# Performance work log

Measured on AMD Instinct MI355X. Metric: run time of the kernel, lower is better.

Reference implementation:

```python
import jax, jax.numpy as jnp
import numpy as np

NUM_ITEMS = 50000
EMB = 16
SLATE = 10
HID = 512
LAT = 64
RESP = 1024
BATCH = 256


def _linear_params(k, out_dim, in_dim):
    kw, kb = jax.random.split(k)
    s = 1.0 / np.sqrt(in_dim)
    W = jax.random.uniform(kw, (out_dim, in_dim), jnp.float32, -s, s)
    b = jax.random.uniform(kb, (out_dim,), jnp.float32, -s, s)
    return W, b


def setup_inputs() -> dict:
    key = jax.random.key(0)
    ks = jax.random.split(key, 10)
    user_repr = jax.random.randint(ks[0], (BATCH, NUM_ITEMS), 0, 2, dtype=jnp.int32)
    slate = jax.random.randint(ks[1], (BATCH, SLATE), 0, NUM_ITEMS, dtype=jnp.int32)
    response_encoded = jax.random.uniform(ks[2], (BATCH, RESP), jnp.float32)
    eps = jax.random.normal(ks[3], (BATCH, LAT), jnp.float32)
    emb = jax.random.normal(ks[4], (NUM_ITEMS, EMB), jnp.float32)
    in_enc = SLATE * EMB + EMB + RESP
    W_enc, b_enc = _linear_params(ks[5], HID, in_enc)
    W_mu, b_mu = _linear_params(ks[6], LAT, HID)
    W_lv, b_lv = _linear_params(ks[7], LAT, HID)
    in_dec = LAT + EMB + RESP
    W_d1, b_d1 = _linear_params(ks[8], HID, in_dec)
    W_d2, b_d2 = _linear_params(ks[9], SLATE * EMB, HID)
    return {"user_repr": user_repr, "slate": slate, "response_encoded": response_encoded,
            "eps": eps, "emb": emb, "W_enc": W_enc, "b_enc": b_enc,
            "W_mu": W_mu, "b_mu": b_mu, "W_lv": W_lv, "b_lv": b_lv,
            "W_d1": W_d1, "b_d1": b_d1, "W_d2": W_d2, "b_d2": b_d2}


def reference(user_repr, slate, response_encoded, eps, emb,
              W_enc, b_enc, W_mu, b_mu, W_lv, b_lv, W_d1, b_d1, W_d2, b_d2):
    # Ragged embedding-mean pooling over interacted items (vectorized segment mean):
    # mean of emb rows where user_repr==1  ==  (indicator @ emb) / count
    uf = user_repr.astype(jnp.float32)                       # [B, N]
    counts = jnp.sum(uf, axis=1, keepdims=True)              # [B, 1]
    user = (uf @ emb) / counts                               # [B, E]

    cond = jnp.concatenate([user, response_encoded], axis=1)  # [B, E+R]
    slate_emb = emb[slate]                                    # [B, K, E]
    slate_vec = slate_emb.reshape(-1, SLATE * EMB)            # [B, K*E]
    x = jnp.concatenate([slate_vec, cond], axis=1)

    # encoder
    h = jax.nn.relu(x @ W_enc.T + b_enc)
    z_mean = h @ W_mu.T + b_mu
    z_log_var = h @ W_lv.T + b_lv

    # reparameterized sample
    z = z_mean + eps * jnp.exp(0.5 * z_log_var)

    # decoder
    dz = jnp.concatenate([z, cond], axis=1)
    dh = jax.nn.relu(dz @ W_d1.T + b_d1)
    rx = jax.nn.relu(dh @ W_d2.T + b_d2)                      # [B, K*E]
    rx = rx.reshape(-1, SLATE, EMB)                           # [B, K, E]

    # scores vs all items, softmax over items
    logits = jnp.einsum('bkh,nh->bkn', rx, emb)               # [B, K, N]
    probs = jax.nn.softmax(logits, axis=2)
    recon_slate = jnp.argmax(probs, axis=2)                   # [B, K]
    recon_resp = jnp.take_along_axis(probs, slate[:, :, None], axis=2)[..., 0]  # [B, K]
    return z_mean, z_log_var, recon_slate, recon_resp
```

## Files before the change

### kernel.cpp

```cpp
#include <hip/hip_runtime.h>

#define NITEMS 50000
#define EMBD   16
#define NSLATE 10
#define HIDD   512
#define LATD   64
#define RESPD  1024
#define BATCH  256
#define NPCH   10
#define PI4    1250
#define BG     4
#define LOG2E  1.44269504088896340736f
#define SHIFT  64.0f

#define NCOL   2560
#define NT     1563
#define IC     128
#define TPC    13

#define OUT_ZM 0
#define OUT_ZLV 16384
#define OUT_RS 32768
#define OUT_RR 35328

#define WS_X    0
#define WS_DZ   307200
#define WS_P2   0
#define WS_PS   0
#define WS_PM   327680
#define WS_PA   655360
#define WS_PP   589824
#define WS_PART 589824
#define WS_RX   1114112
#define WS_RXS0 1155072
#define WS_RXS1 1175552
#define WS_RXS2 1196032

typedef __attribute__((ext_vector_type(8))) short bfrag;
typedef __attribute__((ext_vector_type(16))) float f32x16;

__device__ __forceinline__ float bfround(float v) {
  unsigned u = __float_as_uint(v);
  unsigned r = (u + 0x7FFFu + ((u >> 16) & 1u)) & 0xFFFF0000u;
  return __uint_as_float(r);
}

__global__ __launch_bounds__(256) void pool_part(const int* __restrict__ u,
    const float* __restrict__ emb, float* __restrict__ pp) {
  int bg = blockIdx.x, c = blockIdx.y, t = threadIdx.x;
  float acc[BG][17];
  #pragma unroll
  for (int j = 0; j < BG; ++j)
    #pragma unroll
    for (int i = 0; i < 17; ++i) acc[j][i] = 0.0f;
  const int4* ub = (const int4*)u;
  size_t base = (size_t)(bg * BG) * 12500 + (size_t)c * PI4;
  int nBase = c * 5000;
  for (int i4 = t; i4 < PI4; i4 += 256) {
    int4 u0 = ub[base + i4];
    int4 u1 = ub[base + 12500 + i4];
    int4 u2 = ub[base + 25000 + i4];
    int4 u3 = ub[base + 37500 + i4];
    int w[BG][4] = {{u0.x, u0.y, u0.z, u0.w}, {u1.x, u1.y, u1.z, u1.w},
                    {u2.x, u2.y, u2.z, u2.w}, {u3.x, u3.y, u3.z, u3.w}};
    const float4* e4 = (const float4*)(emb + (size_t)(nBase + i4 * 4) * 16);
    #pragma unroll
    for (int it = 0; it < 4; ++it) {
      float4 ea = e4[it * 4 + 0], eb = e4[it * 4 + 1];
      float4 ec = e4[it * 4 + 2], ed = e4[it * 4 + 3];
      #pragma unroll
      for (int j = 0; j < BG; ++j) {
        float wf = (float)w[j][it];
        acc[j][0]  = fmaf(wf, ea.x, acc[j][0]);
        acc[j][1]  = fmaf(wf, ea.y, acc[j][1]);
        acc[j][2]  = fmaf(wf, ea.z, acc[j][2]);
        acc[j][3]  = fmaf(wf, ea.w, acc[j][3]);
        acc[j][4]  = fmaf(wf, eb.x, acc[j][4]);
        acc[j][5]  = fmaf(wf, eb.y, acc[j][5]);
        acc[j][6]  = fmaf(wf, eb.z, acc[j][6]);
        acc[j][7]  = fmaf(wf, eb.w, acc[j][7]);
        acc[j][8]  = fmaf(wf, ec.x, acc[j][8]);
        acc[j][9]  = fmaf(wf, ec.y, acc[j][9]);
        acc[j][10] = fmaf(wf, ec.z, acc[j][10]);
        acc[j][11] = fmaf(wf, ec.w, acc[j][11]);
        acc[j][12] = fmaf(wf, ed.x, acc[j][12]);
        acc[j][13] = fmaf(wf, ed.y, acc[j][13]);
        acc[j][14] = fmaf(wf, ed.z, acc[j][14]);
        acc[j][15] = fmaf(wf, ed.w, acc[j][15]);
        acc[j][16] += wf;
      }
    }
  }
  #pragma unroll
  for (int off = 32; off > 0; off >>= 1) {
    #pragma unroll
    for (int j = 0; j < BG; ++j)
      #pragma unroll
      for (int i = 0; i < 17; ++i) acc[j][i] += __shfl_down(acc[j][i], off);
  }
  int lane = t & 63, wv = t >> 6;
  if (lane == 0) {
    float* dst = pp + (size_t)((bg * NPCH + c) * 4 + wv) * (BG * 17);
    #pragma unroll
    for (int j = 0; j < BG; ++j)
      #pragma unroll
      for (int i = 0; i < 17; ++i) dst[j * 17 + i] = acc[j][i];
  }
}

__global__ __launch_bounds__(256) void build_x(const float* __restrict__ pp,
    const int* __restrict__ slate, const float* __restrict__ resp,
    const float* __restrict__ emb, float* __restrict__ x, float* __restrict__ dz) {
  __shared__ float fin[17];
  int b = blockIdx.x, t = threadIdx.x;
  if (t < 17) {
    int bg = b >> 2, j = b & 3;
    float a = 0.f;
    const float* p = pp + (size_t)(bg * NPCH * 4) * (BG * 17) + j * 17 + t;
    #pragma unroll
    for (int w = 0; w < NPCH * 4; ++w) a += p[(size_t)w * (BG * 17)];
    fin[t] = a;
  }
  __syncthreads();
  float inv = 1.0f / fin[16];
  if (t < 16) {
    float uv = fin[t] * inv;
    x[b * 1200 + 160 + t] = uv;
    dz[b * 1104 + 64 + t] = uv;
  }
  if (t >= 32 && t < 192) {
    int i = t - 32;
    int k = i >> 4, e = i & 15;
    int it = slate[b * 10 + k];
    x[b * 1200 + i] = emb[(size_t)it * 16 + e];
  }
  for (int i = t; i < 1024; i += 256) {
    float r = resp[b * 1024 + i];
    x[b * 1200 + 176 + i] = r;
    dz[b * 1104 + 80 + i] = r;
  }
}

__global__ __launch_bounds__(256) void gemm64(const float* __restrict__ A,
    const float* __restrict__ B, float* __restrict__ P, int M, int N, int K, int kChunk) {
  __shared__ float As[16][68];
  __shared__ float Bs[16][68];
  int tid = threadIdx.x;
  int m0 = blockIdx.y * 64, n0 = blockIdx.x * 64;
  int ks = blockIdx.z * kChunk;
  int ke = ks + kChunk; if (ke > K) ke = K;
  int sr = tid >> 2;
  int sc = (tid & 3) * 4;
  int tx = tid & 15, ty = tid >> 4;
  float acc[4][4];
  #pragma unroll
  for (int i = 0; i < 4; ++i)
    #pragma unroll
    for (int j = 0; j < 4; ++j) acc[i][j] = 0.f;
  for (int k0 = ks; k0 < ke; k0 += 16) {
    float4 av = make_float4(0.f, 0.f, 0.f, 0.f);
    float4 bv = make_float4(0.f, 0.f, 0.f, 0.f);
    if (k0 + sc < ke)
      av = *(const float4*)(A + (size_t)(m0 + sr) * K + k0 + sc);
    if (k0 + sc < ke && n0 + sr < N)
      bv = *(const float4*)(B + (size_t)(n0 + sr) * K + k0 + sc);
    __syncthreads();
    As[sc][sr] = av.x; As[sc + 1][sr] = av.y; As[sc + 2][sr] = av.z; As[sc + 3][sr] = av.w;
    Bs[sc][sr] = bv.x; Bs[sc + 1][sr] = bv.y; Bs[sc + 2][sr] = bv.z; Bs[sc + 3][sr] = bv.w;
    __syncthreads();
    #pragma unroll
    for (int kk = 0; kk < 16; ++kk) {
      float4 a4 = *(const float4*)&As[kk][4 * ty];
      float4 b4 = *(const float4*)&Bs[kk][4 * tx];
      float a[4] = {a4.x, a4.y, a4.z, a4.w};
      float b[4] = {b4.x, b4.y, b4.z, b4.w};
      #pragma unroll
      for (int i = 0; i < 4; ++i)
        #pragma unroll
        for (int j = 0; j < 4; ++j) acc[i][j] = fmaf(a[i], b[j], acc[i][j]);
    }
  }
  float* Pz = P + (size_t)blockIdx.z * M * N;
  #pragma unroll
  for (int i = 0; i < 4; ++i) {
    int m = m0 + 4 * ty + i, n = n0 + 4 * tx;
    if (n < N)
      *(float4*)(Pz + (size_t)m * N + n) = make_float4(acc[i][0], acc[i][1], acc[i][2], acc[i][3]);
  }
}

__global__ __launch_bounds__(128) void mulv_z_kernel(const float* __restrict__ part,
    const float* __restrict__ benc,
    const float* __restrict__ Wmu, const float* __restrict__ bmu,
    const float* __restrict__ Wlv, const float* __restrict__ blv,
    const float* __restrict__ eps, float* __restrict__ out, float* __restrict__ dz) {
  __shared__ __align__(16) float hs[512];
  __shared__ float zms[64], zlvs[64];
  int b = blockIdx.x, t = threadIdx.x;
  for (int i = t; i < 512; i += 128) {
    float a = benc[i];
    #pragma unroll
    for (int s = 0; s < 4; ++s) a += part[(size_t)s * 131072 + b * 512 + i];
    hs[i] = fmaxf(a, 0.f);
  }
  __syncthreads();
  const float* Wr = (t < 64) ? (Wmu + (size_t)t * 512) : (Wlv + (size_t)(t - 64) * 512);
  float bias = (t < 64) ? bmu[t] : blv[t - 64];
  const float4* w4 = (const float4*)Wr;
  const float4* h4 = (const float4*)hs;
  float a0 = 0.f, a1 = 0.f, a2 = 0.f, a3 = 0.f;
  #pragma unroll 4
  for (int i = 0; i < 128; ++i) {
    float4 w = w4[i], hv = h4[i];
    a0 = fmaf(w.x, hv.x, a0); a1 = fmaf(w.y, hv.y, a1);
    a2 = fmaf(w.z, hv.z, a2); a3 = fmaf(w.w, hv.w, a3);
  }
  float acc = (a0 + a1) + (a2 + a3) + bias;
  if (t < 64) { out[OUT_ZM + b * 64 + t] = acc; zms[t] = acc; }
  else        { out[OUT_ZLV + b * 64 + (t - 64)] = acc; zlvs[t - 64] = acc; }
  __syncthreads();
  if (t < 64) {
    float zv = fmaf(eps[b * 64 + t], __builtin_amdgcn_exp2f(0.7213475204444817f * zlvs[t]), zms[t]);
    dz[b * 1104 + t] = zv;
  }
}

__global__ __launch_bounds__(256) void gemm_d2(const float* __restrict__ part,
    const float* __restrict__ bd1, const float* __restrict__ W, float* __restrict__ p2) {
  __shared__ float As[16][68];
  __shared__ float Bs[16][68];
  const int N = 160;
  int tid = threadIdx.x;
  int m0 = blockIdx.y * 64, n0 = blockIdx.x * 64;
  int ks = blockIdx.z * 64, ke = ks + 64;
  int sr = tid >> 2, sc = (tid & 3) * 4;
  int tx = tid & 15, ty = tid >> 4;
  float acc[4][4];
  #pragma unroll
  for (int i = 0; i < 4; ++i)
    #pragma unroll
    for (int j = 0; j < 4; ++j) acc[i][j] = 0.f;
  for (int k0 = ks; k0 < ke; k0 += 16) {
    int col = k0 + sc;
    const float* p = part + (size_t)(m0 + sr) * 512 + col;
    float4 a0 = *(const float4*)(p);
    float4 a1 = *(const float4*)(p + 131072);
    float4 a2 = *(const float4*)(p + 262144);
    float4 a3 = *(const float4*)(p + 393216);
    float4 bb = *(const float4*)(bd1 + col);
    float4 av;
    av.x = fmaxf(a0.x + a1.x + a2.x + a3.x + bb.x, 0.f);
    av.y = fmaxf(a0.y + a1.y + a2.y + a3.y + bb.y, 0.f);
    av.z = fmaxf(a0.z + a1.z + a2.z + a3.z + bb.z, 0.f);
    av.w = fmaxf(a0.w + a1.w + a2.w + a3.w + bb.w, 0.f);
    float4 bv = make_float4(0.f, 0.f, 0.f, 0.f);
    if (n0 + sr < N)
      bv = *(const float4*)(W + (size_t)(n0 + sr) * 512 + col);
    __syncthreads();
    As[sc][sr] = av.x; As[sc + 1][sr] = av.y; As[sc + 2][sr] = av.z; As[sc + 3][sr] = av.w;
    Bs[sc][sr] = bv.x; Bs[sc + 1][sr] = bv.y; Bs[sc + 2][sr] = bv.z; Bs[sc + 3][sr] = bv.w;
    __syncthreads();
    #pragma unroll
    for (int kk = 0; kk < 16; ++kk) {
      float4 a4 = *(const float4*)&As[kk][4 * ty];
      float4 b4 = *(const float4*)&Bs[kk][4 * tx];
      float a[4] = {a4.x, a4.y, a4.z, a4.w};
      float b[4] = {b4.x, b4.y, b4.z, b4.w};
      #pragma unroll
      for (int i = 0; i < 4; ++i)
        #pragma unroll
        for (int j = 0; j < 4; ++j) acc[i][j] = fmaf(a[i], b[j], acc[i][j]);
    }
  }
  float* Pz = p2 + (size_t)blockIdx.z * 40960;
  #pragma unroll
  for (int i = 0; i < 4; ++i) {
    int m = m0 + 4 * ty + i, n = n0 + 4 * tx;
    if (n < N)
      *(float4*)(Pz + (size_t)m * 160 + n) = make_float4(acc[i][0], acc[i][1], acc[i][2], acc[i][3]);
  }
}

__global__ __launch_bounds__(256) void rx_prep(const float* __restrict__ p2,
    const float* __restrict__ bd2, float* __restrict__ rx,
    unsigned short* __restrict__ rx0, unsigned short* __restrict__ rx1,
    unsigned short* __restrict__ rx2) {
  int b = blockIdx.x, t = threadIdx.x;
  if (t >= 160) return;
  float a = bd2[t];
  #pragma unroll
  for (int z = 0; z < 8; ++z) a += p2[(size_t)z * 40960 + b * 160 + t];
  float v = fmaxf(a, 0.f) * LOG2E;
  rx[b * 160 + t] = v;
  int col = b * 10 + (t >> 4), e = t & 15;
  float f0 = bfround(v);
  float d1 = v - f0;
  float f1 = bfround(d1);
  float d2 = d1 - f1;
  float f2 = bfround(d2);
  rx0[col * 16 + e] = (unsigned short)(__float_as_uint(f0) >> 16);
  rx1[col * 16 + e] = (unsigned short)(__float_as_uint(f1) >> 16);
  rx2[col * 16 + e] = (unsigned short)(__float_as_uint(f2) >> 16);
}

__global__ __launch_bounds__(256) void score_mfma(const float* __restrict__ emb,
    const unsigned short* __restrict__ rx0, const unsigned short* __restrict__ rx1,
    const unsigned short* __restrict__ rx2,
    float* __restrict__ ps, float* __restrict__ pm, int* __restrict__ pa) {
  int t = threadIdx.x;
  int w = t >> 6, l = t & 63;
  int ln = l & 31, hf = l >> 5;
  int pair = blockIdx.x * 4 + w;
  int ic = blockIdx.y;
  int colA = pair * 64 + ln;
  int colB = colA + 32;
  size_t offA = (size_t)colA * 16 + hf * 8;
  size_t offB = (size_t)colB * 16 + hf * 8;
  bfrag bA0 = *(const bfrag*)(rx0 + offA);
  bfrag bA1 = *(const bfrag*)(rx1 + offA);
  bfrag bA2 = *(const bfrag*)(rx2 + offA);
  bfrag bB0 = *(const bfrag*)(rx0 + offB);
  bfrag bB1 = *(const bfrag*)(rx1 + offB);
  bfrag bB2 = *(const bfrag*)(rx2 + offB);
  float sA = 0.f, sB = 0.f;
  float mA = -3.402823466e38f, mB = -3.402823466e38f;
  int aA = 0x7FFFFFFF, aB = 0x7FFFFFFF;
  int ts = ic * TPC, te = ts + TPC;
  if (te > NT) te = NT;
  #pragma unroll 1
  for (int tile = ts; tile < te; ++tile) {
    int r = tile * 32 + ln;
    float4 e0, e1;
    if (r < NITEMS) {
      const float4* p = (const float4*)(emb + (size_t)r * 16 + hf * 8);
      e0 = p[0]; e1 = p[1];
    } else {
      e0 = make_float4(-128.f, -128.f, -128.f, -128.f);
      e1 = e0;
    }
    float ev[8] = {e0.x, e0.y, e0.z, e0.w, e1.x, e1.y, e1.z, e1.w};
    union { bfrag f; unsigned u[4]; } A0, A1, A2;
    #pragma unroll
    for (int j = 0; j < 4; ++j) {
      float v0 = ev[2 * j], v1 = ev[2 * j + 1];
      unsigned u0 = __float_as_uint(v0), u1 = __float_as_uint(v1);
      A0.u[j] = (u0 >> 16) | (u1 & 0xFFFF0000u);
      float r0 = v0 - __uint_as_float(u0 & 0xFFFF0000u);
      float r1 = v1 - __uint_as_float(u1 & 0xFFFF0000u);
      unsigned w0 = __float_as_uint(r0), w1 = __float_as_uint(r1);
      A1.u[j] = (w0 >> 16) | (w1 & 0xFFFF0000u);
      float q0 = r0 - __uint_as_float(w0 & 0xFFFF0000u);
      float q1 = r1 - __uint_as_float(w1 & 0xFFFF0000u);
      A2.u[j] = (__float_as_uint(q0) >> 16) | (__float_as_uint(q1) & 0xFFFF0000u);
    }
    f32x16 accA, accB;
    #pragma unroll
    for (int i = 0; i < 16; ++i) { accA[i] = -SHIFT; accB[i] = -SHIFT; }
    accA = __builtin_amdgcn_mfma_f32_32x32x16_bf16(A1.f, bA1, accA, 0, 0, 0);
    accB = __builtin_amdgcn_mfma_f32_32x32x16_bf16(A1.f, bB1, accB, 0, 0, 0);
    accA = __builtin_amdgcn_mfma_f32_32x32x16_bf16(A2.f, bA0, accA, 0, 0, 0);
    accB = __builtin_amdgcn_mfma_f32_32x32x16_bf16(A2.f, bB0, accB, 0, 0, 0);
    accA = __builtin_amdgcn_mfma_f32_32x32x16_bf16(A0.f, bA2, accA, 0, 0, 0);
    accB = __builtin_amdgcn_mfma_f32_32x32x16_bf16(A0.f, bB2, accB, 0, 0, 0);
    accA = __builtin_amdgcn_mfma_f32_32x32x16_bf16(A1.f, bA0, accA, 0, 0, 0);
    accB = __builtin_amdgcn_mfma_f32_32x32x16_bf16(A1.f, bB0, accB, 0, 0, 0);
    accA = __builtin_amdgcn_mfma_f32_32x32x16_bf16(A0.f, bA1, accA, 0, 0, 0);
    accB = __builtin_amdgcn_mfma_f32_32x32x16_bf16(A0.f, bB1, accB, 0, 0, 0);
    accA = __builtin_amdgcn_mfma_f32_32x32x16_bf16(A0.f, bA0, accA, 0, 0, 0);
    accB = __builtin_amdgcn_mfma_f32_32x32x16_bf16(A0.f, bB0, accB, 0, 0, 0);
    int base = tile * 32 + 4 * hf;
    #pragma unroll
    for (int g = 0; g < 4; ++g) {
      #pragma unroll
      for (int q = 0; q < 4; ++q) {
        int idx = base + 8 * g + q;
        float xa = accA[g * 4 + q];
        sA += __builtin_amdgcn_exp2f(xa);
        if (xa > mA) { mA = xa; aA = idx; }
        float xb = accB[g * 4 + q];
        sB += __builtin_amdgcn_exp2f(xb);
        if (xb > mB) { mB = xb; aB = idx; }
      }
    }
  }
  sA += __shfl_xor(sA, 32);
  sB += __shfl_xor(sB, 32);
  float omA = __shfl_xor(mA, 32); int oaA = __shfl_xor(aA, 32);
  if (omA > mA || (omA == mA && oaA < aA)) { mA = omA; aA = oaA; }
  float omB = __shfl_xor(mB, 32); int oaB = __shfl_xor(aB, 32);
  if (omB > mB || (omB == mB && oaB < aB)) { mB = omB; aB = oaB; }
  if (hf == 0) {
    int idxA = ic * NCOL + colA;
    int idxB = ic * NCOL + colB;
    ps[idxA] = sA; pm[idxA] = mA; pa[idxA] = aA;
    ps[idxB] = sB; pm[idxB] = mB; pa[idxB] = aB;
  }
}

__global__ __launch_bounds__(256) void score_final(const float* __restrict__ psg,
    const float* __restrict__ pmg, const int* __restrict__ pag,
    const float* __restrict__ rx, const float* __restrict__ emb,
    const int* __restrict__ slate, float* __restrict__ out) {
  int tid = blockIdx.x * 256 + threadIdx.x;
  if (tid >= BATCH * 10) return;
  int b = tid / 10, k = tid % 10;
  float S = 0.f, M = -3.402823466e38f;
  int AM = 2147483647;
  for (int c = 0; c < IC; ++c) {
    int idx = c * NCOL + tid;
    S += psg[idx];
    float m2 = pmg[idx];
    int oa = pag[idx];
    bool take = (m2 > M) || (m2 == M && oa < AM);
    AM = take ? oa : AM;
    M = fmaxf(M, m2);
  }
  int it = slate[b * 10 + k];
  const float* er = emb + (size_t)it * 16;
  const float* rr = rx + b * 160 + k * 16;
  float xs = -SHIFT;
  #pragma unroll
  for (int e = 0; e < 16; ++e) xs = fmaf(rr[e], er[e], xs);
  out[OUT_RS + b * 10 + k] = (float)AM;
  out[OUT_RR + b * 10 + k] = __builtin_amdgcn_exp2f(xs) / S;
}

extern "C" void kernel_launch(void* const* d_in, const int* in_sizes, int n_in,
                              void* d_out, int out_size, void* d_ws, size_t ws_size,
                              hipStream_t stream) {
  const int* user_repr = (const int*)d_in[0];
  const int* slate = (const int*)d_in[1];
  const float* resp = (const float*)d_in[2];
  const float* eps = (const float*)d_in[3];
  const float* emb = (const float*)d_in[4];
  const float* W_enc = (const float*)d_in[5];
  const float* b_enc = (const float*)d_in[6];
  const float* W_mu = (const float*)d_in[7];
  const float* b_mu = (const float*)d_in[8];
  const float* W_lv = (const float*)d_in[9];
  const float* b_lv = (const float*)d_in[10];
  const float* W_d1 = (const float*)d_in[11];
  const float* b_d1 = (const float*)d_in[12];
  const float* W_d2 = (const float*)d_in[13];
  const float* b_d2 = (const float*)d_in[14];
  float* out = (float*)d_out;
  float* ws = (float*)d_ws;

  float* x    = ws + WS_X;
  float* dz   = ws + WS_DZ;
  float* p2   = ws + WS_P2;
  float* pp   = ws + WS_PP;
  float* part = ws + WS_PART;
  float* ps   = ws + WS_PS;
  float* pmb  = ws + WS_PM;
  int*   pab  = (int*)(ws + WS_PA);
  float* rx   = ws + WS_RX;
  unsigned short* rx0 = (unsigned short*)(ws + WS_RXS0);
  unsigned short* rx1 = (unsigned short*)(ws + WS_RXS1);
  unsigned short* rx2 = (unsigned short*)(ws + WS_RXS2);

  pool_part<<<dim3(64, NPCH), 256, 0, stream>>>(user_repr, emb, pp);
  build_x<<<256, 256, 0, stream>>>(pp, slate, resp, emb, x, dz);
  gemm64<<<dim3(8, 4, 4), 256, 0, stream>>>(x, W_enc, part, 256, 512, 1200, 300);
  mulv_z_kernel<<<256, 128, 0, stream>>>(part, b_enc, W_mu, b_mu, W_lv, b_lv, eps, out, dz);
  gemm64<<<dim3(8, 4, 4), 256, 0, stream>>>(dz, W_d1, part, 256, 512, 1104, 276);
  gemm_d2<<<dim3(3, 4, 8), 256, 0, stream>>>(part, b_d1, W_d2, p2);
  rx_prep<<<256, 256, 0, stream>>>(p2, b_d2, rx, rx0, rx1, rx2);
  score_mfma<<<dim3(10, IC), 256, 0, stream>>>(emb, rx0, rx1, rx2, ps, pmb, pab);
  score_final<<<10, 256, 0, stream>>>(ps, pmb, pab, rx, emb, slate, out);
}
```

Baseline: 276.1 us.

## Track per-tile max in scoring loop and recover argmax in a fix-up kernel

The score kernel now keeps only the running max value and the tile index that produced it, using a branch-free fmax tree per tile, instead of tracking an element index per element. Per-column results are merged across chunks with 64-bit atomicMax on a packed key of the order-preserving max and the tile index. A new argmax_fix kernel recomputes the winning tile with MFMA to find the exact item index. The item-dimension split also grows from 128 to 224 chunks to raise parallelism. In exchange it adds an extra launch, global atomics, and key zeroing inside rx_prep.

New measurement: 273.0 us. Within noise of the previous version (-1.1%).

```diff
diff --git a/kernel.cpp b/kernel.cpp
--- a/kernel.cpp
+++ b/kernel.cpp
@@ -15,8 +15,8 @@
 
 #define NCOL   2560
 #define NT     1563
-#define IC     128
-#define TPC    13
+#define IC     224
+#define TPC    7
 
 #define OUT_ZM 0
 #define OUT_ZLV 16384
@@ -27,8 +27,7 @@
 #define WS_DZ   307200
 #define WS_P2   0
 #define WS_PS   0
-#define WS_PM   327680
-#define WS_PA   655360
+#define WS_KEY  573440
 #define WS_PP   589824
 #define WS_PART 589824
 #define WS_RX   1114112
@@ -44,6 +43,13 @@
   unsigned r = (u + 0x7FFFu + ((u >> 16) & 1u)) & 0xFFFF0000u;
   return __uint_as_float(r);
 }
+
+__device__ __forceinline__ unsigned mono32(float f) {
+  unsigned u = __float_as_uint(f);
+  return (u & 0x80000000u) ? ~u : (u | 0x80000000u);
+}
+
+#define FMAX3(a, b, c) fmaxf(fmaxf((a), (b)), (c))
 
 __global__ __launch_bounds__(256) void pool_part(const int* __restrict__ u,
     const float* __restrict__ emb, float* __restrict__ pp) {
@@ -284,8 +290,9 @@
 __global__ __launch_bounds__(256) void rx_prep(const float* __restrict__ p2,
     const float* __restrict__ bd2, float* __restrict__ rx,
     unsigned short* __restrict__ rx0, unsigned short* __restrict__ rx1,
-    unsigned short* __restrict__ rx2) {
+    unsigned short* __restrict__ rx2, unsigned long long* __restrict__ keys) {
   int b = blockIdx.x, t = threadIdx.x;
+  if (t < 10) keys[b * 10 + t] = 0ULL;
   if (t >= 160) return;
   float a = bd2[t];
   #pragma unroll
@@ -306,7 +313,7 @@
 __global__ __launch_bounds__(256) void score_mfma(const float* __restrict__ emb,
     const unsigned short* __restrict__ rx0, const unsigned short* __restrict__ rx1,
     const unsigned short* __restrict__ rx2,
-    float* __restrict__ ps, float* __restrict__ pm, int* __restrict__ pa) {
+    float* __restrict__ ps, unsigned long long* __restrict__ keys) {
   int t = threadIdx.x;
   int w = t >> 6, l = t & 63;
   int ln = l & 31, hf = l >> 5;
@@ -324,7 +331,7 @@
   bfrag bB2 = *(const bfrag*)(rx2 + offB);
   float sA = 0.f, sB = 0.f;
   float mA = -3.402823466e38f, mB = -3.402823466e38f;
-  int aA = 0x7FFFFFFF, aB = 0x7FFFFFFF;
+  int tlA = 0, tlB = 0;
   int ts = ic * TPC, te = ts + TPC;
   if (te > NT) te = NT;
   #pragma unroll 1
@@ -368,60 +375,140 @@
     accB = __builtin_amdgcn_mfma_f32_32x32x16_bf16(A0.f, bB1, accB, 0, 0, 0);
     accA = __builtin_amdgcn_mfma_f32_32x32x16_bf16(A0.f, bA0, accA, 0, 0, 0);
     accB = __builtin_amdgcn_mfma_f32_32x32x16_bf16(A0.f, bB0, accB, 0, 0, 0);
-    int base = tile * 32 + 4 * hf;
-    #pragma unroll
-    for (int g = 0; g < 4; ++g) {
-      #pragma unroll
-      for (int q = 0; q < 4; ++q) {
-        int idx = base + 8 * g + q;
-        float xa = accA[g * 4 + q];
-        sA += __builtin_amdgcn_exp2f(xa);
-        if (xa > mA) { mA = xa; aA = idx; }
-        float xb = accB[g * 4 + q];
-        sB += __builtin_amdgcn_exp2f(xb);
-        if (xb > mB) { mB = xb; aB = idx; }
-      }
+    float tmA, tmB;
+    {
+      float f1 = FMAX3(accA[0], accA[1], accA[2]);
+      float f2 = FMAX3(accA[3], accA[4], accA[5]);
+      float f3 = FMAX3(accA[6], accA[7], accA[8]);
+      float f4 = FMAX3(accA[9], accA[10], accA[11]);
+      float f5 = FMAX3(accA[12], accA[13], accA[14]);
+      float g1 = FMAX3(f1, f2, accA[15]);
+      float g2 = fmaxf(f3, f4);
+      tmA = FMAX3(g1, g2, f5);
+    }
+    {
+      float f1 = FMAX3(accB[0], accB[1], accB[2]);
+      float f2 = FMAX3(accB[3], accB[4], accB[5]);
+      float f3 = FMAX3(accB[6], accB[7], accB[8]);
+      float f4 = FMAX3(accB[9], accB[10], accB[11]);
+      float f5 = FMAX3(accB[12], accB[13], accB[14]);
+      float g1 = FMAX3(f1, f2, accB[15]);
+      float g2 = fmaxf(f3, f4);
+      tmB = FMAX3(g1, g2, f5);
+    }
+    if (tmA > mA) { mA = tmA; tlA = tile; }
+    if (tmB > mB) { mB = tmB; tlB = tile; }
+    #pragma unroll
+    for (int i = 0; i < 16; ++i) {
+      sA += __builtin_amdgcn_exp2f(accA[i]);
+      sB += __builtin_amdgcn_exp2f(accB[i]);
     }
   }
   sA += __shfl_xor(sA, 32);
   sB += __shfl_xor(sB, 32);
-  float omA = __shfl_xor(mA, 32); int oaA = __shfl_xor(aA, 32);
-  if (omA > mA || (omA == mA && oaA < aA)) { mA = omA; aA = oaA; }
-  float omB = __shfl_xor(mB, 32); int oaB = __shfl_xor(aB, 32);
-  if (omB > mB || (omB == mB && oaB < aB)) { mB = omB; aB = oaB; }
+  {
+    float om = __shfl_xor(mA, 32); int ot = __shfl_xor(tlA, 32);
+    if (om > mA || (om == mA && ot < tlA)) { mA = om; tlA = ot; }
+  }
+  {
+    float om = __shfl_xor(mB, 32); int ot = __shfl_xor(tlB, 32);
+    if (om > mB || (om == mB && ot < tlB)) { mB = om; tlB = ot; }
+  }
   if (hf == 0) {
-    int idxA = ic * NCOL + colA;
-    int idxB = ic * NCOL + colB;
-    ps[idxA] = sA; pm[idxA] = mA; pa[idxA] = aA;
-    ps[idxB] = sB; pm[idxB] = mB; pa[idxB] = aB;
+    ps[ic * NCOL + colA] = sA;
+    ps[ic * NCOL + colB] = sB;
+    unsigned long long kA = ((unsigned long long)mono32(mA) << 32) | (unsigned)(2047 - tlA);
+    unsigned long long kB = ((unsigned long long)mono32(mB) << 32) | (unsigned)(2047 - tlB);
+    if (kA > keys[colA]) atomicMax(&keys[colA], kA);
+    if (kB > keys[colB]) atomicMax(&keys[colB], kB);
+  }
+}
+
+__global__ __launch_bounds__(64) void argmax_fix(const unsigned long long* __restrict__ keys,
+    const unsigned short* __restrict__ rx0, const unsigned short* __restrict__ rx1,
+    const unsigned short* __restrict__ rx2, const float* __restrict__ emb,
+    float* __restrict__ out) {
+  int l = threadIdx.x, ln = l & 31, hf = l >> 5;
+  int g = blockIdx.x, k = blockIdx.y;
+  int col = g * 32 + ln;
+  unsigned long long key = keys[col];
+  unsigned um = (unsigned)(key >> 32);
+  int tl = 2047 - (int)(key & 0xFFFFFFFFu);
+  size_t off = (size_t)col * 16 + hf * 8;
+  bfrag b0 = *(const bfrag*)(rx0 + off);
+  bfrag b1 = *(const bfrag*)(rx1 + off);
+  bfrag b2 = *(const bfrag*)(rx2 + off);
+  bool done = ((tl & 7) != k);
+  while (true) {
+    int tsel = done ? 0x7FFFFFFF : tl;
+    #pragma unroll
+    for (int o = 32; o > 0; o >>= 1) tsel = min(tsel, __shfl_xor(tsel, o));
+    if (tsel == 0x7FFFFFFF) break;
+    int r = tsel * 32 + ln;
+    float4 e0, e1;
+    if (r < NITEMS) {
+      const float4* p = (const float4*)(emb + (size_t)r * 16 + hf * 8);
+      e0 = p[0]; e1 = p[1];
+    } else {
+      e0 = make_float4(-128.f, -128.f, -128.f, -128.f);
+      e1 = e0;
+    }
+    float ev[8] = {e0.x, e0.y, e0.z, e0.w, e1.x, e1.y, e1.z, e1.w};
+    union { bfrag f; unsigned u[4]; } A0, A1, A2;
+    #pragma unroll
+    for (int j = 0; j < 4; ++j) {
+      float v0 = ev[2 * j], v1 = ev[2 * j + 1];
+      unsigned u0 = __float_as_uint(v0), u1 = __float_as_uint(v1);
+      A0.u[j] = (u0 >> 16) | (u1 & 0xFFFF0000u);
+      float r0 = v0 - __uint_as_float(u0 & 0xFFFF0000u);
+      float r1 = v1 - __uint_as_float(u1 & 0xFFFF0000u);
+      unsigned w0 = __float_as_uint(r0), w1 = __float_as_uint(r1);
+      A1.u[j] = (w0 >> 16) | (w1 & 0xFFFF0000u);
+      float q0 = r0 - __uint_as_float(w0 & 0xFFFF0000u);
+      float q1 = r1 - __uint_as_float(w1 & 0xFFFF0000u);
+      A2.u[j] = (__float_as_uint(q0) >> 16) | (__float_as_uint(q1) & 0xFFFF0000u);
+    }
+    f32x16 acc;
+    #pragma unroll
+    for (int i = 0; i < 16; ++i) acc[i] = -SHIFT;
+    acc = __builtin_amdgcn_mfma_f32_32x32x16_bf16(A1.f, b1, acc, 0, 0, 0);
+    acc = __builtin_amdgcn_mfma_f32_32x32x16_bf16(A2.f, b0, acc, 0, 0, 0);
+    acc = __builtin_amdgcn_mfma_f32_32x32x16_bf16(A0.f, b2, acc, 0, 0, 0);
+    acc = __builtin_amdgcn_mfma_f32_32x32x16_bf16(A1.f, b0, acc, 0, 0, 0);
+    acc = __builtin_amdgcn_mfma_f32_32x32x16_bf16(A0.f, b1, acc, 0, 0, 0);
+    acc = __builtin_amdgcn_mfma_f32_32x32x16_bf16(A0.f, b0, acc, 0, 0, 0);
+    if (!done && tl == tsel) {
+      int best = 0x7FFFFFFF;
+      #pragma unroll
+      for (int g2 = 0; g2 < 4; ++g2)
+        #pragma unroll
+        for (int i = 0; i < 4; ++i) {
+          float x = acc[g2 * 4 + i];
+          int row = 8 * g2 + 4 * hf + i;
+          if (mono32(x) == um) best = min(best, tsel * 32 + row);
+        }
+      int ob = __shfl_xor(best, 32);
+      best = min(best, ob);
+      if (hf == 0) out[OUT_RS + col] = (float)best;
+      done = true;
+    }
   }
 }
 
 __global__ __launch_bounds__(256) void score_final(const float* __restrict__ psg,
-    const float* __restrict__ pmg, const int* __restrict__ pag,
     const float* __restrict__ rx, const float* __restrict__ emb,
     const int* __restrict__ slate, float* __restrict__ out) {
   int tid = blockIdx.x * 256 + threadIdx.x;
   if (tid >= BATCH * 10) return;
   int b = tid / 10, k = tid % 10;
-  float S = 0.f, M = -3.402823466e38f;
-  int AM = 2147483647;
-  for (int c = 0; c < IC; ++c) {
-    int idx = c * NCOL + tid;
-    S += psg[idx];
-    float m2 = pmg[idx];
-    int oa = pag[idx];
-    bool take = (m2 > M) || (m2 == M && oa < AM);
-    AM = take ? oa : AM;
-    M = fmaxf(M, m2);
-  }
+  float S = 0.f;
+  for (int c = 0; c < IC; ++c) S += psg[c * NCOL + tid];
   int it = slate[b * 10 + k];
   const float* er = emb + (size_t)it * 16;
   const float* rr = rx + b * 160 + k * 16;
   float xs = -SHIFT;
   #pragma unroll
   for (int e = 0; e < 16; ++e) xs = fmaf(rr[e], er[e], xs);
-  out[OUT_RS + b * 10 + k] = (float)AM;
   out[OUT_RR + b * 10 + k] = __builtin_amdgcn_exp2f(xs) / S;
 }
 
@@ -452,8 +539,7 @@
   float* pp   = ws + WS_PP;
   float* part = ws + WS_PART;
   float* ps   = ws + WS_PS;
-  float* pmb  = ws + WS_PM;
-  int*   pab  = (int*)(ws + WS_PA);
+  unsigned long long* keys = (unsigned long long*)(ws + WS_KEY);
   float* rx   = ws + WS_RX;
   unsigned short* rx0 = (unsigned short*)(ws + WS_RXS0);
   unsigned short* rx1 = (unsigned short*)(ws + WS_RXS1);
@@ -465,7 +551,8 @@
   mulv_z_kernel<<<256, 128, 0, stream>>>(part, b_enc, W_mu, b_mu, W_lv, b_lv, eps, out, dz);
   gemm64<<<dim3(8, 4, 4), 256, 0, stream>>>(dz, W_d1, part, 256, 512, 1104, 276);
   gemm_d2<<<dim3(3, 4, 8), 256, 0, stream>>>(part, b_d1, W_d2, p2);
-  rx_prep<<<256, 256, 0, stream>>>(p2, b_d2, rx, rx0, rx1, rx2);
-  score_mfma<<<dim3(10, IC), 256, 0, stream>>>(emb, rx0, rx1, rx2, ps, pmb, pab);
-  score_final<<<10, 256, 0, stream>>>(ps, pmb, pab, rx, emb, slate, out);
-}
+  rx_prep<<<256, 256, 0, stream>>>(p2, b_d2, rx, rx0, rx1, rx2, keys);
+  score_mfma<<<dim3(10, IC), 256, 0, stream>>>(emb, rx0, rx1, rx2, ps, keys);
+  argmax_fix<<<dim3(80, 8), 64, 0, stream>>>(keys, rx0, rx1, rx2, emb, out);
+  score_final<<<10, 256, 0, stream>>>(ps, rx, emb, slate, out);
+}
```
